# Kernel tuning notes

Hardware: AMD Instinct MI355X
Metric: run time of the kernel (lower is better)

The kernel has to match this reference:

```python
import jax, jax.numpy as jnp
import numpy as np
import math

N_QUBITS = 6
N_LAYERS = 3
OUT_DIM = 8
B = 131072
F = 24


def _gate_rx(a):
    # RX(a) = [[cos(a/2), -i sin(a/2)], [-i sin(a/2), cos(a/2)]]; a: scalar or [B]
    c = jnp.cos(a / 2).astype(jnp.complex64)
    s = (-1j * jnp.sin(a / 2)).astype(jnp.complex64)
    return jnp.stack([jnp.stack([c, s], -1), jnp.stack([s, c], -1)], -2)


def _gate_ry(a):
    c = jnp.cos(a / 2).astype(jnp.complex64)
    s = jnp.sin(a / 2).astype(jnp.complex64)
    return jnp.stack([jnp.stack([c, -s], -1), jnp.stack([s, c], -1)], -2)


def _gate_rz(a):
    # RZ(a) = diag(e^{-ia/2}, e^{ia/2})
    e = jnp.exp(-0.5j * a.astype(jnp.complex64))
    z = jnp.zeros_like(e)
    return jnp.stack([jnp.stack([e, z], -1), jnp.stack([z, jnp.conj(e)], -1)], -2)


def _apply_1q(state, gate, q, batched):
    # state: [B] + [2]*N_QUBITS ; gate: [2,2] or [B,2,2]
    s = jnp.moveaxis(state, 1 + q, 1)
    if batched:
        out = jnp.einsum('bij,bj...->bi...', gate, s)
    else:
        out = jnp.einsum('ij,bj...->bi...', gate, s)
    return jnp.moveaxis(out, 1, 1 + q)


def _apply_cnot(state, c, t):
    # flip target where control bit == 1
    cax = 1 + c
    s0 = jnp.take(state, 0, axis=cax)
    s1 = jnp.take(state, 1, axis=cax)
    tax = 1 + t if t < c else t  # control axis removed
    s1 = jnp.flip(s1, axis=tax)
    return jnp.stack([s0, s1], axis=cax)


def _circuit(x, theta):
    Bn = x.shape[0]
    # pooling branch of forward: chunks of size ceil(F/n_qubits)=4, mean each
    x_packed = x.reshape(Bn, N_QUBITS, F // N_QUBITS).mean(-1)
    angles = jnp.clip(x_packed, -6.0, 6.0) / 6.0 * math.pi  # [B, n_qubits]

    state = jnp.zeros((Bn,) + (2,) * N_QUBITS, dtype=jnp.complex64)
    state = state.at[(slice(None),) + (0,) * N_QUBITS].set(1.0)

    # angle encoding: RX(a_q), RZ(0.5*a_q) per qubit (batched gates)
    for q in range(N_QUBITS):
        state = _apply_1q(state, _gate_rx(angles[:, q]), q, batched=True)
        state = _apply_1q(state, _gate_rz(0.5 * angles[:, q]), q, batched=True)

    for l in range(N_LAYERS):
        for q in range(N_QUBITS - 1):
            state = _apply_cnot(state, q, q + 1)
        state = _apply_cnot(state, N_QUBITS - 1, 0)
        for q in range(N_QUBITS):
            state = _apply_1q(state, _gate_rx(theta[l, q, 0]), q, batched=False)
            state = _apply_1q(state, _gate_ry(theta[l, q, 1]), q, batched=False)
            state = _apply_1q(state, _gate_rz(theta[l, q, 2]), q, batched=False)

    probs = jnp.abs(state) ** 2  # real
    meas = []
    for k in range(OUT_DIM):
        q = k % N_QUBITS
        if k % 2 == 0:  # PauliZ
            pq = jnp.sum(probs, axis=tuple(a for a in range(1, N_QUBITS + 1) if a != 1 + q))
            meas.append(pq[:, 0] - pq[:, 1])
        else:  # PauliX: Re <psi| X_q |psi>
            flipped = jnp.flip(state, axis=1 + q)
            meas.append(jnp.real(jnp.sum(jnp.conj(state) * flipped, axis=tuple(range(1, N_QUBITS + 1)))))
    return jnp.stack(meas, axis=1).astype(jnp.float32)  # [B, out_dim]


def setup_inputs() -> dict:
    key = jax.random.key(0)
    k1, k2 = jax.random.split(key)
    x = jax.random.normal(k1, (B, F), dtype=jnp.float32)
    theta = jax.random.normal(k2, (N_LAYERS, N_QUBITS, 3), dtype=jnp.float32) * 0.1
    return {"x": x, "theta": theta}


def reference(x, theta):
    return _circuit(x, theta)
```

## Files before the change

kernel.cpp:

```cpp
#include <hip/hip_runtime.h>
#include <math.h>


typedef _Float16 half8v __attribute__((ext_vector_type(8)));
typedef __fp16   fp16x2 __attribute__((ext_vector_type(2)));
typedef float    float4v __attribute__((ext_vector_type(4)));

__device__ __forceinline__ float2 pk_cmul(float2 g, float2 a) {
    float2 t;
    asm("v_pk_mul_f32 %0, %1, %2 op_sel:[0,0] op_sel_hi:[0,1]"
        : "=v"(t) : "v"(g), "v"(a));
    asm("v_pk_fma_f32 %0, %1, %2, %0 op_sel:[1,1,0] op_sel_hi:[1,0,1] neg_lo:[1,0,0]"
        : "+v"(t) : "v"(g), "v"(a));
    return t;
}
__device__ __forceinline__ float2 pk_cmac(float2 acc, float2 g, float2 a) {
    asm("v_pk_fma_f32 %0, %1, %2, %0 op_sel:[0,0,0] op_sel_hi:[0,1,1]"
        : "+v"(acc) : "v"(g), "v"(a));
    asm("v_pk_fma_f32 %0, %1, %2, %0 op_sel:[1,1,0] op_sel_hi:[1,0,1] neg_lo:[1,0,0]"
        : "+v"(acc) : "v"(g), "v"(a));
    return acc;
}

__device__ __forceinline__ float xpair(float v) {
    return __int_as_float(__builtin_amdgcn_mov_dpp(__float_as_int(v), 0xB1, 0xF, 0xF, true));
}
__device__ __forceinline__ float2 xpair2(float2 v) {
    return make_float2(xpair(v.x), xpair(v.y));
}

template<int M>
__device__ __forceinline__ void apply1q(float2* st, float2 g00, float2 g01,
                                        float2 g10, float2 g11) {
#pragma unroll
    for (int j = 0; j < 32; ++j) {
        if (j & M) continue;
        float2 a = st[j], b = st[j + M];
        float2 na = pk_cmul(g00, a); na = pk_cmac(na, g01, b);
        float2 nb = pk_cmul(g10, a); nb = pk_cmac(nb, g11, b);
        st[j] = na; st[j + M] = nb;
    }
}

template<int MC, int MT>
__device__ __forceinline__ void cnot(float2* st) {
#pragma unroll
    for (int j = 0; j < 32; ++j) {
        if ((j & MC) && !(j & MT)) {
            float2 tmp = st[j]; st[j] = st[j + MT]; st[j + MT] = tmp;
        }
    }
}

struct cf { float r, i; };
__device__ __forceinline__ cf scmul(cf a, cf b) {
    return { fmaf(a.r, b.r, -a.i * b.i), fmaf(a.r, b.i, a.i * b.r) };
}

__device__ __forceinline__ int rpos(int row, int k) {
    return ((((row >> 4) * 4 + (k >> 5)) * 4 + ((k >> 3) & 3)) * 16 + (row & 15)) * 8 + (k & 7);
}

__device__ __forceinline__ int permrow(int a) {
    return (((a >> 4) & 1) << 5) | (((a >> 2) & 1) << 4) | (((a >> 5) & 1) << 3)
         | (((a >> 3) & 1) << 2) | ((a & 1) << 1) | ((a >> 1) & 1);
}

__global__ __launch_bounds__(128) void ubuild_kernel(
    const float* __restrict__ theta, float* __restrict__ Rw) {
    __shared__ float2 gs[18 * 4];
    __shared__ float Rls[16384];
    const int t = threadIdx.x;
    if (t < 18) {
        const float* th = theta + t * 3;
        float sx, cx, sy, cy, sz, cz;
        __sincosf(0.5f * th[0], &sx, &cx);
        __sincosf(0.5f * th[1], &sy, &cy);
        __sincosf(0.5f * th[2], &sz, &cz);
        cf m00 = {  cy * cx,  sy * sx };
        cf m01 = { -sy * cx, -cy * sx };
        cf m10 = {  sy * cx, -cy * sx };
        cf m11 = {  cy * cx, -sy * sx };
        cf e0 = { cz, -sz }, e1 = { cz, sz };
        cf g00 = scmul(e0, m00), g01 = scmul(e0, m01);
        cf g10 = scmul(e1, m10), g11 = scmul(e1, m11);
        float2* o = gs + t * 4;
        o[0] = make_float2(g00.r, g00.i);
        o[1] = make_float2(g01.r, g01.i);
        o[2] = make_float2(g10.r, g10.i);
        o[3] = make_float2(g11.r, g11.i);
    }
    __syncthreads();

    const int c  = t >> 1;
    const bool pb = (t & 1) != 0;

    const int  target = c & 31;
    const bool mine   = ((c >> 5) == (pb ? 1 : 0));
    float2 st[32];
#pragma unroll
    for (int j = 0; j < 32; ++j)
        st[j] = make_float2((mine && j == target) ? 1.f : 0.f, 0.f);

#pragma unroll 1
    for (int l = 0; l < 3; ++l) {
#pragma unroll
        for (int j = 0; j < 16; ++j) {
            float2 lo = st[j], hi = st[j + 16];
            st[j].x      = pb ? hi.x : lo.x;  st[j].y      = pb ? hi.y : lo.y;
            st[j + 16].x = pb ? lo.x : hi.x;  st[j + 16].y = pb ? lo.y : hi.y;
        }
        cnot<16, 8>(st);
        cnot< 8, 4>(st);
        cnot< 4, 2>(st);
        cnot< 2, 1>(st);
#pragma unroll
        for (int j = 1; j < 32; j += 2) st[j] = xpair2(st[j]);

        const float2* g = gs + l * 24;
        {
            float2 q00 = g[0], q01 = g[1], q10 = g[2], q11 = g[3];
            float2 gm, go;
            gm.x = pb ? q11.x : q00.x;  gm.y = pb ? q11.y : q00.y;
            go.x = pb ? q10.x : q01.x;  go.y = pb ? q10.y : q01.y;
#pragma unroll
            for (int j = 0; j < 32; ++j) {
                float2 other = xpair2(st[j]);
                float2 nv = pk_cmul(gm, st[j]);
                st[j] = pk_cmac(nv, go, other);
            }
        }
        apply1q<16>(st, g[ 4], g[ 5], g[ 6], g[ 7]);
        apply1q< 8>(st, g[ 8], g[ 9], g[10], g[11]);
        apply1q< 4>(st, g[12], g[13], g[14], g[15]);
        apply1q< 2>(st, g[16], g[17], g[18], g[19]);
        apply1q< 1>(st, g[20], g[21], g[22], g[23]);
    }

#pragma unroll
    for (int j = 0; j < 32; ++j) {
        const int a  = (pb ? 32 : 0) + j;
        const int pr = permrow(a);
        const float re = st[j].x, im = st[j].y;
        Rls[rpos(pr,      c)]      =  re;
        Rls[rpos(pr,      c + 64)] = -im;
        Rls[rpos(pr + 64, c)]      =  im;
        Rls[rpos(pr + 64, c + 64)] =  re;
    }
    __syncthreads();

    unsigned short* hiw = (unsigned short*)Rw;
    unsigned short* low = hiw + 16384;
#pragma unroll 1
    for (int n = 0; n < 16; ++n) {
        const int base = n * 1024 + t * 8;
        half8v hv, lv;
#pragma unroll
        for (int u = 0; u < 8; ++u) {
            float xx = Rls[base + u];
            _Float16 hh = (_Float16)xx;
            hv[u] = hh;
            lv[u] = (_Float16)(xx - (float)hh);
        }
        *reinterpret_cast<half8v*>(hiw + base) = hv;
        *reinterpret_cast<half8v*>(low + base) = lv;
    }
}

__device__ __forceinline__ void encode_elem(const float* __restrict__ xptr,
                                            int h, half8v* bh, half8v* bl) {
    const float4* xv = reinterpret_cast<const float4*>(xptr);
    float2 v0[6], v1[6];
#pragma unroll
    for (int q = 0; q < 6; ++q) {
        float4 xq = xv[q];
        float m = (xq.x + xq.y + xq.z + xq.w) * 0.25f;
        m = fminf(fmaxf(m, -6.0f), 6.0f);
        float a = m * 0.52359877559829887308f;
        float s4, c4;
        __sincosf(0.25f * a, &s4, &c4);
        float s2 = 2.f * s4 * c4;
        float c2 = fmaf(-2.f * s4, s4, 1.f);
        v0[q] = make_float2(c4 * c2, -s4 * c2);
        v1[q] = make_float2(s4 * s2, -c4 * s2);
    }
    float2 u01[4], T[8];
    u01[0] = pk_cmul(v0[4], v0[5]);
    u01[1] = pk_cmul(v0[4], v1[5]);
    u01[2] = pk_cmul(v1[4], v0[5]);
    u01[3] = pk_cmul(v1[4], v1[5]);
#pragma unroll
    for (int j = 0; j < 8; ++j)
        T[j] = pk_cmul((j & 4) ? v1[3] : v0[3], u01[j & 3]);
    float2 Q  = pk_cmul((h & 2) ? v1[1] : v0[1], (h & 1) ? v1[2] : v0[2]);
    float2 P1 = pk_cmul(v0[0], Q);
    float2 P2 = pk_cmul(v1[0], Q);

#pragma unroll
    for (int j = 0; j < 8; j += 2) {
        float2 a1a = pk_cmul(P1, T[j]), a1b = pk_cmul(P1, T[j + 1]);
        float2 a2a = pk_cmul(P2, T[j]), a2b = pk_cmul(P2, T[j + 1]);
#define SPLIT(S, va, vb)                                                      \
        {                                                                     \
            fp16x2 hp = __builtin_amdgcn_cvt_pkrtz(va, vb);                   \
            fp16x2 lp = __builtin_amdgcn_cvt_pkrtz(va - (float)hp[0],         \
                                                   vb - (float)hp[1]);        \
            bh[S][j] = (_Float16)hp[0]; bh[S][j + 1] = (_Float16)hp[1];       \
            bl[S][j] = (_Float16)lp[0]; bl[S][j + 1] = (_Float16)lp[1];       \
        }
        SPLIT(0, a1a.x, a1b.x)
        SPLIT(1, a2a.x, a2b.x)
        SPLIT(2, a1a.y, a1b.y)
        SPLIT(3, a2a.y, a2b.y)
#undef SPLIT
    }
}

__device__ __forceinline__ void measure_store(const float4v* acc, int h,
                                              float* __restrict__ outp) {
    float tot = 0.f, z4 = 0.f, x1 = 0.f, x3 = 0.f, x5 = 0.f;
#pragma unroll
    for (int m = 0; m < 4; ++m)
#pragma unroll
        for (int r = 0; r < 4; ++r) {
            float re = acc[m][r], im = acc[m + 4][r];
            float p = fmaf(re, re, im * im);
            tot += p;
            z4 += (r & 1) ? -p : p;
        }
#pragma unroll
    for (int m = 0; m < 2; ++m)
#pragma unroll
        for (int r = 0; r < 4; ++r)
            x1 += fmaf(acc[m][r], acc[m + 2][r], acc[m + 4][r] * acc[m + 6][r]);
#pragma unroll
    for (int m = 0; m < 4; m += 2)
#pragma unroll
        for (int r = 0; r < 4; ++r)
            x3 += fmaf(acc[m][r], acc[m + 1][r], acc[m + 4][r] * acc[m + 5][r]);
#pragma unroll
    for (int m = 0; m < 4; ++m)
#pragma unroll
        for (int r = 0; r < 2; ++r)
            x5 += fmaf(acc[m][r], acc[m][r + 2], acc[m + 4][r] * acc[m + 4][r + 2]);

    float z0 = (h & 2) ? -tot : tot;
    float z2 = (h & 1) ? -tot : tot;

#pragma unroll
    for (int d = 16; d <= 32; d <<= 1) {
        z0 += __shfl_xor(z0, d, 64);
        z2 += __shfl_xor(z2, d, 64);
        z4 += __shfl_xor(z4, d, 64);
        x1 += __shfl_xor(x1, d, 64);
        x3 += __shfl_xor(x3, d, 64);
        x5 += __shfl_xor(x5, d, 64);
    }
    x1 *= 2.f; x3 *= 2.f; x5 *= 2.f;

    if (h == 0)
        *reinterpret_cast<float4*>(outp) = make_float4(z0, x1, z2, x3);
    else if (h == 1)
        *reinterpret_cast<float4*>(outp + 4) = make_float4(z4, x5, z0, x1);
}

__global__ __launch_bounds__(256) void qsim2_kernel(
    const float* __restrict__ x, const float* __restrict__ Rg,
    float* __restrict__ out) {
    __shared__ __align__(16) unsigned short Abuf[32768];
    const int t = threadIdx.x;

    {
        const float4* g4 = reinterpret_cast<const float4*>(Rg);
#pragma unroll
        for (int ii = 0; ii < 16; ++ii) {
            const float4* gp = g4 + ii * 256 + t;
            unsigned short* lp = Abuf + ii * 2048 + (t >> 6) * 512;
            __builtin_amdgcn_global_load_lds(
                (const __attribute__((address_space(1))) unsigned int*)gp,
                (__attribute__((address_space(3))) unsigned int*)lp, 16, 0, 0);
        }
    }

    const int l = t & 63, w = t >> 6;
    const int e16 = l & 15, h = l >> 4;
    const int elem0 = (blockIdx.x * 4 + w) * 32 + e16;
    const int elem1 = elem0 + 16;

    half8v b0h[4], b0l[4], b1h[4], b1l[4];
    encode_elem(x + (size_t)elem0 * 24, h, b0h, b0l);
    encode_elem(x + (size_t)elem1 * 24, h, b1h, b1l);

    __syncthreads();

    float4v acc0[8], acc1[8];
#pragma unroll
    for (int m = 0; m < 8; ++m) {
        acc0[m] = (float4v){0.f, 0.f, 0.f, 0.f};
        acc1[m] = (float4v){0.f, 0.f, 0.f, 0.f};
    }
#pragma unroll
    for (int m = 0; m < 8; ++m) {
#pragma unroll
        for (int s = 0; s < 4; ++s) {
            const int fo = ((m * 4 + s) * 64 + l) * 8;
            half8v ah = *reinterpret_cast<const half8v*>(&Abuf[fo]);
            half8v al = *reinterpret_cast<const half8v*>(&Abuf[16384 + fo]);
            acc0[m] = __builtin_amdgcn_mfma_f32_16x16x32_f16(ah, b0h[s], acc0[m], 0, 0, 0);
            acc1[m] = __builtin_amdgcn_mfma_f32_16x16x32_f16(ah, b1h[s], acc1[m], 0, 0, 0);
            acc0[m] = __builtin_amdgcn_mfma_f32_16x16x32_f16(ah, b0l[s], acc0[m], 0, 0, 0);
            acc1[m] = __builtin_amdgcn_mfma_f32_16x16x32_f16(ah, b1l[s], acc1[m], 0, 0, 0);
            acc0[m] = __builtin_amdgcn_mfma_f32_16x16x32_f16(al, b0h[s], acc0[m], 0, 0, 0);
            acc1[m] = __builtin_amdgcn_mfma_f32_16x16x32_f16(al, b1h[s], acc1[m], 0, 0, 0);
        }
    }

    measure_store(acc0, h, out + (size_t)elem0 * 8);
    measure_store(acc1, h, out + (size_t)elem1 * 8);
}

extern "C" void kernel_launch(void* const* d_in, const int* in_sizes, int n_in,
                              void* d_out, int out_size, void* d_ws, size_t ws_size,
                              hipStream_t stream) {
    const float* x     = (const float*)d_in[0];
    const float* theta = (const float*)d_in[1];
    float* out = (float*)d_out;
    float* R   = (float*)d_ws;
    const int B = in_sizes[0] / 24;
    ubuild_kernel<<<dim3(1), dim3(128), 0, stream>>>(theta, R);
    qsim2_kernel<<<dim3(B / 128), dim3(256), 0, stream>>>(x, R, out);
}
```

Baseline: 85.83 us.

## Fuse unitary construction into main kernel, rebuilding it per block in LDS

Removes the separate single-block kernel that built the circuit unitary into workspace and instead has every block of the main kernel compute the 3-layer unitary with 128 threads and write its fp16 hi/lo split directly into shared memory. This eliminates a kernel launch, the serial dependency between the two kernels, and the global round trip of the matrix. In exchange every block repeats the gate-application work, adding per-block latency before the MFMA phase.

```diff
diff --git a/kernel.cpp b/kernel.cpp
--- a/kernel.cpp
+++ b/kernel.cpp
@@ -66,11 +66,110 @@
          | (((a >> 3) & 1) << 2) | ((a & 1) << 1) | ((a >> 1) & 1);
 }
 
-__global__ __launch_bounds__(128) void ubuild_kernel(
-    const float* __restrict__ theta, float* __restrict__ Rw) {
+__device__ __forceinline__ void encode_elem(const float* __restrict__ xptr,
+                                            int h, half8v* bh, half8v* bl) {
+    const float4* xv = reinterpret_cast<const float4*>(xptr);
+    float2 v0[6], v1[6];
+#pragma unroll
+    for (int q = 0; q < 6; ++q) {
+        float4 xq = xv[q];
+        float m = (xq.x + xq.y + xq.z + xq.w) * 0.25f;
+        m = fminf(fmaxf(m, -6.0f), 6.0f);
+        float a = m * 0.52359877559829887308f;
+        float s4, c4;
+        __sincosf(0.25f * a, &s4, &c4);
+        float s2 = 2.f * s4 * c4;
+        float c2 = fmaf(-2.f * s4, s4, 1.f);
+        v0[q] = make_float2(c4 * c2, -s4 * c2);
+        v1[q] = make_float2(s4 * s2, -c4 * s2);
+    }
+    float2 u01[4], T[8];
+    u01[0] = pk_cmul(v0[4], v0[5]);
+    u01[1] = pk_cmul(v0[4], v1[5]);
+    u01[2] = pk_cmul(v1[4], v0[5]);
+    u01[3] = pk_cmul(v1[4], v1[5]);
+#pragma unroll
+    for (int j = 0; j < 8; ++j)
+        T[j] = pk_cmul((j & 4) ? v1[3] : v0[3], u01[j & 3]);
+    float2 Q  = pk_cmul((h & 2) ? v1[1] : v0[1], (h & 1) ? v1[2] : v0[2]);
+    float2 P1 = pk_cmul(v0[0], Q);
+    float2 P2 = pk_cmul(v1[0], Q);
+
+#pragma unroll
+    for (int j = 0; j < 8; j += 2) {
+        float2 a1a = pk_cmul(P1, T[j]), a1b = pk_cmul(P1, T[j + 1]);
+        float2 a2a = pk_cmul(P2, T[j]), a2b = pk_cmul(P2, T[j + 1]);
+#define SPLIT(S, va, vb)                                                      \
+        {                                                                     \
+            fp16x2 hp = __builtin_amdgcn_cvt_pkrtz(va, vb);                   \
+            fp16x2 lp = __builtin_amdgcn_cvt_pkrtz(va - (float)hp[0],         \
+                                                   vb - (float)hp[1]);        \
+            bh[S][j] = (_Float16)hp[0]; bh[S][j + 1] = (_Float16)hp[1];       \
+            bl[S][j] = (_Float16)lp[0]; bl[S][j + 1] = (_Float16)lp[1];       \
+        }
+        SPLIT(0, a1a.x, a1b.x)
+        SPLIT(1, a2a.x, a2b.x)
+        SPLIT(2, a1a.y, a1b.y)
+        SPLIT(3, a2a.y, a2b.y)
+#undef SPLIT
+    }
+}
+
+__device__ __forceinline__ void measure_store(const float4v* acc, int h,
+                                              float* __restrict__ outp) {
+    float tot = 0.f, z4 = 0.f, x1 = 0.f, x3 = 0.f, x5 = 0.f;
+#pragma unroll
+    for (int m = 0; m < 4; ++m)
+#pragma unroll
+        for (int r = 0; r < 4; ++r) {
+            float re = acc[m][r], im = acc[m + 4][r];
+            float p = fmaf(re, re, im * im);
+            tot += p;
+            z4 += (r & 1) ? -p : p;
+        }
+#pragma unroll
+    for (int m = 0; m < 2; ++m)
+#pragma unroll
+        for (int r = 0; r < 4; ++r)
+            x1 += fmaf(acc[m][r], acc[m + 2][r], acc[m + 4][r] * acc[m + 6][r]);
+#pragma unroll
+    for (int m = 0; m < 4; m += 2)
+#pragma unroll
+        for (int r = 0; r < 4; ++r)
+            x3 += fmaf(acc[m][r], acc[m + 1][r], acc[m + 4][r] * acc[m + 5][r]);
+#pragma unroll
+    for (int m = 0; m < 4; ++m)
+#pragma unroll
+        for (int r = 0; r < 2; ++r)
+            x5 += fmaf(acc[m][r], acc[m][r + 2], acc[m + 4][r] * acc[m + 4][r + 2]);
+
+    float z0 = (h & 2) ? -tot : tot;
+    float z2 = (h & 1) ? -tot : tot;
+
+#pragma unroll
+    for (int d = 16; d <= 32; d <<= 1) {
+        z0 += __shfl_xor(z0, d, 64);
+        z2 += __shfl_xor(z2, d, 64);
+        z4 += __shfl_xor(z4, d, 64);
+        x1 += __shfl_xor(x1, d, 64);
+        x3 += __shfl_xor(x3, d, 64);
+        x5 += __shfl_xor(x5, d, 64);
+    }
+    x1 *= 2.f; x3 *= 2.f; x5 *= 2.f;
+
+    if (h == 0)
+        *reinterpret_cast<float4*>(outp) = make_float4(z0, x1, z2, x3);
+    else if (h == 1)
+        *reinterpret_cast<float4*>(outp + 4) = make_float4(z4, x5, z0, x1);
+}
+
+__global__ __launch_bounds__(256) void qsim_fused_kernel(
+    const float* __restrict__ x, const float* __restrict__ theta,
+    float* __restrict__ out) {
     __shared__ float2 gs[18 * 4];
-    __shared__ float Rls[16384];
+    __shared__ __align__(16) _Float16 Abuf[32768];
     const int t = threadIdx.x;
+
     if (t < 18) {
         const float* th = theta + t * 3;
         float sx, cx, sy, cy, sz, cz;
@@ -92,193 +191,69 @@
     }
     __syncthreads();
 
-    const int c  = t >> 1;
-    const bool pb = (t & 1) != 0;
-
-    const int  target = c & 31;
-    const bool mine   = ((c >> 5) == (pb ? 1 : 0));
-    float2 st[32];
-#pragma unroll
-    for (int j = 0; j < 32; ++j)
-        st[j] = make_float2((mine && j == target) ? 1.f : 0.f, 0.f);
+    if (t < 128) {
+        const int c  = t >> 1;
+        const bool pb = (t & 1) != 0;
+
+        const int  target = c & 31;
+        const bool mine   = ((c >> 5) == (pb ? 1 : 0));
+        float2 st[32];
+#pragma unroll
+        for (int j = 0; j < 32; ++j)
+            st[j] = make_float2((mine && j == target) ? 1.f : 0.f, 0.f);
 
 #pragma unroll 1
-    for (int l = 0; l < 3; ++l) {
-#pragma unroll
-        for (int j = 0; j < 16; ++j) {
-            float2 lo = st[j], hi = st[j + 16];
-            st[j].x      = pb ? hi.x : lo.x;  st[j].y      = pb ? hi.y : lo.y;
-            st[j + 16].x = pb ? lo.x : hi.x;  st[j + 16].y = pb ? lo.y : hi.y;
-        }
-        cnot<16, 8>(st);
-        cnot< 8, 4>(st);
-        cnot< 4, 2>(st);
-        cnot< 2, 1>(st);
-#pragma unroll
-        for (int j = 1; j < 32; j += 2) st[j] = xpair2(st[j]);
-
-        const float2* g = gs + l * 24;
-        {
-            float2 q00 = g[0], q01 = g[1], q10 = g[2], q11 = g[3];
-            float2 gm, go;
-            gm.x = pb ? q11.x : q00.x;  gm.y = pb ? q11.y : q00.y;
-            go.x = pb ? q10.x : q01.x;  go.y = pb ? q10.y : q01.y;
-#pragma unroll
-            for (int j = 0; j < 32; ++j) {
-                float2 other = xpair2(st[j]);
-                float2 nv = pk_cmul(gm, st[j]);
-                st[j] = pk_cmac(nv, go, other);
+        for (int l = 0; l < 3; ++l) {
+#pragma unroll
+            for (int j = 0; j < 16; ++j) {
+                float2 lo = st[j], hi = st[j + 16];
+                st[j].x      = pb ? hi.x : lo.x;  st[j].y      = pb ? hi.y : lo.y;
+                st[j + 16].x = pb ? lo.x : hi.x;  st[j + 16].y = pb ? lo.y : hi.y;
             }
-        }
-        apply1q<16>(st, g[ 4], g[ 5], g[ 6], g[ 7]);
-        apply1q< 8>(st, g[ 8], g[ 9], g[10], g[11]);
-        apply1q< 4>(st, g[12], g[13], g[14], g[15]);
-        apply1q< 2>(st, g[16], g[17], g[18], g[19]);
-        apply1q< 1>(st, g[20], g[21], g[22], g[23]);
-    }
-
-#pragma unroll
-    for (int j = 0; j < 32; ++j) {
-        const int a  = (pb ? 32 : 0) + j;
-        const int pr = permrow(a);
-        const float re = st[j].x, im = st[j].y;
-        Rls[rpos(pr,      c)]      =  re;
-        Rls[rpos(pr,      c + 64)] = -im;
-        Rls[rpos(pr + 64, c)]      =  im;
-        Rls[rpos(pr + 64, c + 64)] =  re;
-    }
-    __syncthreads();
-
-    unsigned short* hiw = (unsigned short*)Rw;
-    unsigned short* low = hiw + 16384;
-#pragma unroll 1
-    for (int n = 0; n < 16; ++n) {
-        const int base = n * 1024 + t * 8;
-        half8v hv, lv;
-#pragma unroll
-        for (int u = 0; u < 8; ++u) {
-            float xx = Rls[base + u];
-            _Float16 hh = (_Float16)xx;
-            hv[u] = hh;
-            lv[u] = (_Float16)(xx - (float)hh);
-        }
-        *reinterpret_cast<half8v*>(hiw + base) = hv;
-        *reinterpret_cast<half8v*>(low + base) = lv;
-    }
-}
-
-__device__ __forceinline__ void encode_elem(const float* __restrict__ xptr,
-                                            int h, half8v* bh, half8v* bl) {
-    const float4* xv = reinterpret_cast<const float4*>(xptr);
-    float2 v0[6], v1[6];
-#pragma unroll
-    for (int q = 0; q < 6; ++q) {
-        float4 xq = xv[q];
-        float m = (xq.x + xq.y + xq.z + xq.w) * 0.25f;
-        m = fminf(fmaxf(m, -6.0f), 6.0f);
-        float a = m * 0.52359877559829887308f;
-        float s4, c4;
-        __sincosf(0.25f * a, &s4, &c4);
-        float s2 = 2.f * s4 * c4;
-        float c2 = fmaf(-2.f * s4, s4, 1.f);
-        v0[q] = make_float2(c4 * c2, -s4 * c2);
-        v1[q] = make_float2(s4 * s2, -c4 * s2);
-    }
-    float2 u01[4], T[8];
-    u01[0] = pk_cmul(v0[4], v0[5]);
-    u01[1] = pk_cmul(v0[4], v1[5]);
-    u01[2] = pk_cmul(v1[4], v0[5]);
-    u01[3] = pk_cmul(v1[4], v1[5]);
-#pragma unroll
-    for (int j = 0; j < 8; ++j)
-        T[j] = pk_cmul((j & 4) ? v1[3] : v0[3], u01[j & 3]);
-    float2 Q  = pk_cmul((h & 2) ? v1[1] : v0[1], (h & 1) ? v1[2] : v0[2]);
-    float2 P1 = pk_cmul(v0[0], Q);
-    float2 P2 = pk_cmul(v1[0], Q);
-
-#pragma unroll
-    for (int j = 0; j < 8; j += 2) {
-        float2 a1a = pk_cmul(P1, T[j]), a1b = pk_cmul(P1, T[j + 1]);
-        float2 a2a = pk_cmul(P2, T[j]), a2b = pk_cmul(P2, T[j + 1]);
-#define SPLIT(S, va, vb)                                                      \
-        {                                                                     \
-            fp16x2 hp = __builtin_amdgcn_cvt_pkrtz(va, vb);                   \
-            fp16x2 lp = __builtin_amdgcn_cvt_pkrtz(va - (float)hp[0],         \
-                                                   vb - (float)hp[1]);        \
-            bh[S][j] = (_Float16)hp[0]; bh[S][j + 1] = (_Float16)hp[1];       \
-            bl[S][j] = (_Float16)lp[0]; bl[S][j + 1] = (_Float16)lp[1];       \
-        }
-        SPLIT(0, a1a.x, a1b.x)
-        SPLIT(1, a2a.x, a2b.x)
-        SPLIT(2, a1a.y, a1b.y)
-        SPLIT(3, a2a.y, a2b.y)
-#undef SPLIT
-    }
-}
-
-__device__ __forceinline__ void measure_store(const float4v* acc, int h,
-                                              float* __restrict__ outp) {
-    float tot = 0.f, z4 = 0.f, x1 = 0.f, x3 = 0.f, x5 = 0.f;
-#pragma unroll
-    for (int m = 0; m < 4; ++m)
-#pragma unroll
-        for (int r = 0; r < 4; ++r) {
-            float re = acc[m][r], im = acc[m + 4][r];
-            float p = fmaf(re, re, im * im);
-            tot += p;
-            z4 += (r & 1) ? -p : p;
-        }
-#pragma unroll
-    for (int m = 0; m < 2; ++m)
-#pragma unroll
-        for (int r = 0; r < 4; ++r)
-            x1 += fmaf(acc[m][r], acc[m + 2][r], acc[m + 4][r] * acc[m + 6][r]);
-#pragma unroll
-    for (int m = 0; m < 4; m += 2)
-#pragma unroll
-        for (int r = 0; r < 4; ++r)
-            x3 += fmaf(acc[m][r], acc[m + 1][r], acc[m + 4][r] * acc[m + 5][r]);
-#pragma unroll
-    for (int m = 0; m < 4; ++m)
-#pragma unroll
-        for (int r = 0; r < 2; ++r)
-            x5 += fmaf(acc[m][r], acc[m][r + 2], acc[m + 4][r] * acc[m + 4][r + 2]);
-
-    float z0 = (h & 2) ? -tot : tot;
-    float z2 = (h & 1) ? -tot : tot;
-
-#pragma unroll
-    for (int d = 16; d <= 32; d <<= 1) {
-        z0 += __shfl_xor(z0, d, 64);
-        z2 += __shfl_xor(z2, d, 64);
-        z4 += __shfl_xor(z4, d, 64);
-        x1 += __shfl_xor(x1, d, 64);
-        x3 += __shfl_xor(x3, d, 64);
-        x5 += __shfl_xor(x5, d, 64);
-    }
-    x1 *= 2.f; x3 *= 2.f; x5 *= 2.f;
-
-    if (h == 0)
-        *reinterpret_cast<float4*>(outp) = make_float4(z0, x1, z2, x3);
-    else if (h == 1)
-        *reinterpret_cast<float4*>(outp + 4) = make_float4(z4, x5, z0, x1);
-}
-
-__global__ __launch_bounds__(256) void qsim2_kernel(
-    const float* __restrict__ x, const float* __restrict__ Rg,
-    float* __restrict__ out) {
-    __shared__ __align__(16) unsigned short Abuf[32768];
-    const int t = threadIdx.x;
-
-    {
-        const float4* g4 = reinterpret_cast<const float4*>(Rg);
-#pragma unroll
-        for (int ii = 0; ii < 16; ++ii) {
-            const float4* gp = g4 + ii * 256 + t;
-            unsigned short* lp = Abuf + ii * 2048 + (t >> 6) * 512;
-            __builtin_amdgcn_global_load_lds(
-                (const __attribute__((address_space(1))) unsigned int*)gp,
-                (__attribute__((address_space(3))) unsigned int*)lp, 16, 0, 0);
+            cnot<16, 8>(st);
+            cnot< 8, 4>(st);
+            cnot< 4, 2>(st);
+            cnot< 2, 1>(st);
+#pragma unroll
+            for (int j = 1; j < 32; j += 2) st[j] = xpair2(st[j]);
+
+            const float2* g = gs + l * 24;
+            {
+                float2 q00 = g[0], q01 = g[1], q10 = g[2], q11 = g[3];
+                float2 gm, go;
+                gm.x = pb ? q11.x : q00.x;  gm.y = pb ? q11.y : q00.y;
+                go.x = pb ? q10.x : q01.x;  go.y = pb ? q10.y : q01.y;
+#pragma unroll
+                for (int j = 0; j < 32; ++j) {
+                    float2 other = xpair2(st[j]);
+                    float2 nv = pk_cmul(gm, st[j]);
+                    st[j] = pk_cmac(nv, go, other);
+                }
+            }
+            apply1q<16>(st, g[ 4], g[ 5], g[ 6], g[ 7]);
+            apply1q< 8>(st, g[ 8], g[ 9], g[10], g[11]);
+            apply1q< 4>(st, g[12], g[13], g[14], g[15]);
+            apply1q< 2>(st, g[16], g[17], g[18], g[19]);
+            apply1q< 1>(st, g[20], g[21], g[22], g[23]);
+        }
+
+        _Float16* hiB = Abuf;
+        _Float16* loB = Abuf + 16384;
+#pragma unroll
+        for (int j = 0; j < 32; ++j) {
+            const int a  = (pb ? 32 : 0) + j;
+            const int pr = permrow(a);
+            const float re = st[j].x, im = st[j].y;
+            _Float16 hr = (_Float16)re;  _Float16 lr = (_Float16)(re - (float)hr);
+            _Float16 hm = (_Float16)im;  _Float16 lm = (_Float16)(im - (float)hm);
+            const int p00 = rpos(pr,      c);
+            const int p01 = rpos(pr,      c + 64);
+            const int p10 = rpos(pr + 64, c);
+            const int p11 = rpos(pr + 64, c + 64);
+            hiB[p00] =  hr;  loB[p00] =  lr;
+            hiB[p01] = -hm;  loB[p01] = -lm;
+            hiB[p10] =  hm;  loB[p10] =  lm;
+            hiB[p11] =  hr;  loB[p11] =  lr;
         }
     }
 
@@ -325,8 +300,6 @@
     const float* x     = (const float*)d_in[0];
     const float* theta = (const float*)d_in[1];
     float* out = (float*)d_out;
-    float* R   = (float*)d_ws;
     const int B = in_sizes[0] / 24;
-    ubuild_kernel<<<dim3(1), dim3(128), 0, stream>>>(theta, R);
-    qsim2_kernel<<<dim3(B / 128), dim3(256), 0, stream>>>(x, R, out);
-}
+    qsim_fused_kernel<<<dim3(B / 128), dim3(256), 0, stream>>>(x, theta, out);
+}
```

New measurement: 114.5 us. 33.4% more time.
